# Optimization experiments

Measured on AMD Instinct MI355X. Metric: run time of the kernel, lower is better.

Reference implementation:

```python
import jax, jax.numpy as jnp
import numpy as np

B, T, P, H, D = 2, 2048, 1024, 16, 128
C = H * D  # 2048
ROPE_THETA = 10000.0


def setup_inputs() -> dict:
    key = jax.random.key(0)
    ks = jax.random.split(key, 5)
    x = jax.random.normal(ks[0], (B, T, C), jnp.float32)
    w_qkv = jax.random.normal(ks[1], (C, 3 * C), jnp.float32) * 0.02  # Linear(dim, 3*dim), applied as x @ w
    w_out = jax.random.normal(ks[2], (C, C), jnp.float32) * 0.02
    past_k = jax.random.normal(ks[3], (B, H, P, D), jnp.float32)
    past_v = jax.random.normal(ks[4], (B, H, P, D), jnp.float32)
    return {"x": x, "w_qkv": w_qkv, "w_out": w_out, "past_k": past_k, "past_v": past_v}


def _rope(q, k, offset):
    # rotate-half RoPE (GPT-NeoX style), positions offset..offset+T-1
    d = q.shape[-1]
    inv_freq = 1.0 / (ROPE_THETA ** (jnp.arange(0, d, 2, dtype=jnp.float32) / d))  # [d/2]
    pos = offset + jnp.arange(q.shape[2], dtype=jnp.float32)                        # [T]
    ang = pos[:, None] * inv_freq[None, :]                                          # [T, d/2]
    cos = jnp.concatenate([jnp.cos(ang), jnp.cos(ang)], -1)[None, None]             # [1,1,T,d]
    sin = jnp.concatenate([jnp.sin(ang), jnp.sin(ang)], -1)[None, None]

    def rot_half(t):
        t1, t2 = jnp.split(t, 2, axis=-1)
        return jnp.concatenate([-t2, t1], -1)

    return q * cos + rot_half(q) * sin, k * cos + rot_half(k) * sin


def reference(x, w_qkv, w_out, past_k, past_v):
    Bv, Tv, Cv = x.shape
    Hn = past_k.shape[1]
    Dd = Cv // Hn
    # fused QKV projection
    qkv = x @ w_qkv                       # [B,T,3C]
    q, k, v = jnp.split(qkv, 3, axis=-1)  # each [B,T,C]

    def split_heads(t):
        return t.reshape(Bv, Tv, Hn, Dd).transpose(0, 2, 1, 3)  # [B,H,T,D]

    q, k, v = split_heads(q), split_heads(k), split_heads(v)
    # RoPE with offset = past length
    q, k = _rope(q, k, past_k.shape[2])
    # KV-cache concat along time axis
    k = jnp.concatenate([past_k, k], axis=2)  # [B,H,P+T,D]
    v = jnp.concatenate([past_v, v], axis=2)
    # SDPA: past_kv present -> is_causal=False, no mask (full attention)
    scale = 1.0 / jnp.sqrt(jnp.float32(Dd))
    scores = jnp.einsum('bhqd,bhkd->bhqk', q, k) * scale
    attn = jax.nn.softmax(scores, axis=-1)
    out = jnp.einsum('bhqk,bhkd->bhqd', attn, v)
    out = out.transpose(0, 2, 1, 3).reshape(Bv, Tv, Cv)
    return out @ w_out
```

## Files before the change

kernel.cpp:

```cpp
#include <hip/hip_runtime.h>
#include <stdint.h>

#define B_ 2
#define T_ 2048
#define P_ 1024
#define H_ 16
#define D_ 128
#define C_ 2048
#define S_ 3072
#define M_ 4096
#define N3_ 6144

typedef unsigned short u16;
typedef unsigned int uint32;
typedef __attribute__((ext_vector_type(8))) short short8;
typedef __attribute__((ext_vector_type(8))) __bf16 bf16x8;
typedef __attribute__((ext_vector_type(4))) float f32x4;
typedef __attribute__((ext_vector_type(16))) float f32x16;
typedef __attribute__((ext_vector_type(4))) unsigned short u16x4;
typedef __attribute__((ext_vector_type(4))) unsigned int uint4v;

static __device__ __forceinline__ float bf2f(u16 h) {
    union { unsigned int u; float f; } x; x.u = ((unsigned int)h) << 16; return x.f;
}
static __device__ __forceinline__ u16 f2bf(float f) {
    return __builtin_bit_cast(u16, (__bf16)f);
}
static __device__ __forceinline__ uint32 pkbf(float x, float y) {
    return (uint32)f2bf(x) | ((uint32)f2bf(y) << 16);
}

static __device__ __forceinline__ f32x4 mfma_bf16(short8 a, short8 b, f32x4 c) {
    return __builtin_amdgcn_mfma_f32_16x16x32_bf16(
        __builtin_bit_cast(bf16x8, a), __builtin_bit_cast(bf16x8, b), c, 0, 0, 0);
}
static __device__ __forceinline__ f32x16 mfma32(short8 a, short8 b, f32x16 c) {
    return __builtin_amdgcn_mfma_f32_32x32x16_bf16(
        __builtin_bit_cast(bf16x8, a), __builtin_bit_cast(bf16x8, b), c, 0, 0, 0);
}

typedef __attribute__((address_space(3))) unsigned int lds_u32;
typedef const __attribute__((address_space(1))) unsigned int glb_u32;
static __device__ __forceinline__ void gload_lds16(const void* g, void* l) {
    __builtin_amdgcn_global_load_lds((glb_u32*)g, (lds_u32*)l, 16, 0, 0);
}

static __device__ __forceinline__ void storeC(float* p, float v) { *p = v; }
static __device__ __forceinline__ void storeC(u16* p, float v) { *p = f2bf(v); }


__global__ void castx_kernel(const float* __restrict__ x, u16* __restrict__ Xb) {
    int idx = blockIdx.x * 256 + threadIdx.x;
    const float4 v = ((const float4*)x)[idx];
    u16x4 o;
    o.x = f2bf(v.x); o.y = f2bf(v.y); o.z = f2bf(v.z); o.w = f2bf(v.w);
    ((u16x4*)Xb)[idx] = o;
}

__global__ void wT_kernel(const float* __restrict__ W, u16* __restrict__ Wt,
                          int Ndim, int Kdim) {
    __shared__ float tile[64][65];
    const int n0 = blockIdx.x * 64, k0 = blockIdx.y * 64;
    const int tid = threadIdx.x;
#pragma unroll
    for (int i = 0; i < 16; i++) {
        int idx = tid + i * 256;
        int r = idx >> 6, c = idx & 63;
        tile[r][c] = W[(size_t)(k0 + r) * Ndim + n0 + c];
    }
    __syncthreads();
#pragma unroll
    for (int i = 0; i < 16; i++) {
        int idx = tid + i * 256;
        int r = idx >> 6, c = idx & 63;
        Wt[(size_t)(n0 + r) * Kdim + k0 + c] = f2bf(tile[c][r]);
    }
}

__global__ void rope_table_kernel(float* __restrict__ cosT, float* __restrict__ sinT) {
    int idx = blockIdx.x * 256 + threadIdx.x;
    int t = idx >> 6, d = idx & 63;
    float inv = powf(10000.0f, -(float)d * (1.0f / 64.0f));
    float ang = (float)(P_ + t) * inv;
    cosT[idx] = cosf(ang);
    sinT[idx] = sinf(ang);
}

__global__ void rope_qk_kernel(u16* __restrict__ QKVb, u16* __restrict__ Kc,
                               const float* __restrict__ cosT,
                               const float* __restrict__ sinT) {
    int idx = blockIdx.x * 256 + threadIdx.x;
    int d = idx & 63;
    int h = (idx >> 6) & 15;
    int t = (idx >> 10) & 2047;
    int b = idx >> 21;
    size_t rowoff = (size_t)(b * T_ + t) * N3_;
    float c = cosT[(t << 6) + d], s = sinT[(t << 6) + d];
    {
        u16* p1 = QKVb + rowoff + h * 128 + d;
        float x1 = bf2f(p1[0]), x2 = bf2f(p1[64]);
        p1[0]  = f2bf(x1 * c - x2 * s);
        p1[64] = f2bf(x2 * c + x1 * s);
    }
    {
        const u16* p1 = QKVb + rowoff + C_ + h * 128 + d;
        float x1 = bf2f(p1[0]), x2 = bf2f(p1[64]);
        u16* o = Kc + ((size_t)(b * H_ + h) * S_ + P_ + t) * 128 + d;
        o[0]  = f2bf(x1 * c - x2 * s);
        o[64] = f2bf(x2 * c + x1 * s);
    }
}

__global__ void pastk_kernel(const float* __restrict__ past_k, u16* __restrict__ Kc) {
    int idx = blockIdx.x * 256 + threadIdx.x;
    int d = idx & 127;
    int p = (idx >> 7) & 1023;
    int bh = idx >> 17;
    Kc[((size_t)bh * S_ + p) * 128 + d] = f2bf(past_k[idx]);
}

__global__ void vnewT_kernel(const u16* __restrict__ QKVb, u16* __restrict__ Vt) {
    __shared__ u16 tile[64][65];
    const int t0 = blockIdx.x * 64, d0 = blockIdx.y * 64, bh = blockIdx.z;
    const int b = bh >> 4, h = bh & 15;
    const int tid = threadIdx.x;
#pragma unroll
    for (int i = 0; i < 16; i++) {
        int idx = tid + i * 256;
        int r = idx >> 6, c = idx & 63;
        tile[r][c] = QKVb[(size_t)(b * T_ + t0 + r) * N3_ + 2 * C_ + h * 128 + d0 + c];
    }
    __syncthreads();
#pragma unroll
    for (int i = 0; i < 16; i++) {
        int idx = tid + i * 256;
        int r = idx >> 6, c = idx & 63;
        Vt[((size_t)bh * 128 + d0 + r) * S_ + P_ + t0 + c] = tile[c][r];
    }
}

__global__ void vpastT_kernel(const float* __restrict__ past_v, u16* __restrict__ Vt) {
    __shared__ float tile[64][65];
    const int p0 = blockIdx.x * 64, d0 = blockIdx.y * 64, bh = blockIdx.z;
    const int tid = threadIdx.x;
#pragma unroll
    for (int i = 0; i < 16; i++) {
        int idx = tid + i * 256;
        int r = idx >> 6, c = idx & 63;
        tile[r][c] = past_v[((size_t)bh * P_ + p0 + r) * 128 + d0 + c];
    }
    __syncthreads();
#pragma unroll
    for (int i = 0; i < 16; i++) {
        int idx = tid + i * 256;
        int r = idx >> 6, c = idx & 63;
        Vt[((size_t)bh * 128 + d0 + r) * S_ + p0 + c] = f2bf(tile[c][r]);
    }
}

template <typename OutT>
__global__ void __launch_bounds__(512, 1)
gemm3(const u16* __restrict__ A, const u16* __restrict__ Bt,
      OutT* __restrict__ Co, int Mdim, int Ndim, int Kdim) {
    __shared__ u16 lA[3 * 256 * 64];
    __shared__ u16 lB[3 * 128 * 64];
    const int nbx = Ndim >> 7;
    const int nwg = (Mdim >> 8) * nbx;
    int bid = blockIdx.x;
    int wg = (bid & 7) * (nwg >> 3) + (bid >> 3);
    const int bm = wg / nbx, bn = wg % nbx;
    const int m0 = bm << 8, n0 = bn << 7;
    const int tid = threadIdx.x;
    const int wave = tid >> 6, lane = tid & 63;
    const int mw = wave >> 1, nw = wave & 1;
    const int l15 = lane & 15, l4 = lane >> 4;

    f32x4 acc[4][4];
#pragma unroll
    for (int i = 0; i < 4; i++)
#pragma unroll
        for (int j = 0; j < 4; j++) acc[i][j] = (f32x4){0.f, 0.f, 0.f, 0.f};

    const u16* aSrc[4];
    const u16* bSrc[2];
#pragma unroll
    for (int i = 0; i < 4; i++) {
        int cid = i * 512 + tid;
        int r = cid >> 3, pc = cid & 7;
        aSrc[i] = A + (size_t)(m0 + r) * Kdim + ((pc ^ (r & 7)) << 3);
    }
#pragma unroll
    for (int i = 0; i < 2; i++) {
        int cid = i * 512 + tid;
        int r = cid >> 3, pc = cid & 7;
        bSrc[i] = Bt + (size_t)(n0 + r) * Kdim + ((pc ^ (r & 7)) << 3);
    }

#define STAGE3(bi, kt) do {                                                     \
    u16* _pa = lA + (bi) * 16384 + wave * 512;                                  \
    u16* _pb = lB + (bi) * 8192 + wave * 512;                                   \
    _Pragma("unroll")                                                           \
    for (int i = 0; i < 4; i++)                                                 \
        gload_lds16(aSrc[i] + (size_t)(kt) * 64, _pa + i * 4096);               \
    _Pragma("unroll")                                                           \
    for (int i = 0; i < 2; i++)                                                 \
        gload_lds16(bSrc[i] + (size_t)(kt) * 64, _pb + i * 4096);               \
} while (0)

    STAGE3(0, 0);
    STAGE3(1, 1);

    const int NT = Kdim >> 6;
    int bc = 0;
    for (int t = 0; t < NT; ++t) {
        if (t + 1 < NT) asm volatile("s_waitcnt vmcnt(6)" ::: "memory");
        else            asm volatile("s_waitcnt vmcnt(0)" ::: "memory");
        __builtin_amdgcn_s_barrier();
        asm volatile("" ::: "memory");
        if (t + 2 < NT) {
            int b2 = bc + 2; if (b2 >= 3) b2 -= 3;
            STAGE3(b2, t + 2);
        }
        const u16* la = lA + bc * 16384;
        const u16* lb = lB + bc * 8192;
        short8 af[4][2], bf[4][2];
#pragma unroll
        for (int i = 0; i < 4; i++)
#pragma unroll
            for (int kk = 0; kk < 2; kk++) {
                int r = mw * 64 + i * 16 + l15;
                int cb = (kk * 64 + l4 * 16) ^ ((r & 7) << 4);
                af[i][kk] = *(const short8*)&la[r * 64 + (cb >> 1)];
            }
#pragma unroll
        for (int j = 0; j < 4; j++)
#pragma unroll
            for (int kk = 0; kk < 2; kk++) {
                int r = nw * 64 + j * 16 + l15;
                int cb = (kk * 64 + l4 * 16) ^ ((r & 7) << 4);
                bf[j][kk] = *(const short8*)&lb[r * 64 + (cb >> 1)];
            }
        __builtin_amdgcn_s_setprio(1);
#pragma unroll
        for (int kk = 0; kk < 2; kk++)
#pragma unroll
            for (int i = 0; i < 4; i++)
#pragma unroll
                for (int j = 0; j < 4; j++)
                    acc[i][j] = mfma_bf16(af[i][kk], bf[j][kk], acc[i][j]);
        __builtin_amdgcn_s_setprio(0);
        __builtin_amdgcn_sched_barrier(0);
        bc = bc + 1; if (bc >= 3) bc = 0;
    }
#undef STAGE3

#pragma unroll
    for (int i = 0; i < 4; i++)
#pragma unroll
        for (int j = 0; j < 4; j++) {
            int row = m0 + mw * 64 + i * 16 + (l4 << 2);
            int col = n0 + nw * 64 + j * 16 + l15;
#pragma unroll
            for (int q = 0; q < 4; q++)
                storeC(&Co[(size_t)(row + q) * Ndim + col], acc[i][j][q]);
        }
}

__global__ void __launch_bounds__(256, 2)
attn_kernel(const u16* __restrict__ QKVb, const u16* __restrict__ Kc,
            const u16* __restrict__ Vt, u16* __restrict__ O) {
    __shared__ u16 ldsK[2][64 * 128];
    __shared__ u16 ldsV[2][128 * 64];

    int bid = blockIdx.x;
    int wg = (bid & 7) * 64 + (bid >> 3);
    const int qc = wg & 15;
    const int bh = wg >> 4;
    const int b = bh >> 4, h = bh & 15;
    const int tid = threadIdx.x, wave = tid >> 6, lane = tid & 63;
    const int l31 = lane & 31, hi = lane >> 5;

    const int krow = tid >> 4;
    const int kcol = (((tid & 15) << 4) ^ ((krow & 7) << 4)) >> 1;
    const int vrow = tid >> 3;
    const int vcol = (((tid & 7) << 4) ^ ((vrow & 7) << 4)) >> 1;

    const u16* Kbh = Kc + (size_t)bh * S_ * 128;
    const u16* Vbh = Vt + (size_t)bh * 128 * S_;

    const int tq = qc * 128 + wave * 32 + l31;
    short8 qf[8];
    {
        const u16* qp = QKVb + (size_t)(b * T_ + tq) * N3_ + h * 128 + hi * 8;
#pragma unroll
        for (int ks = 0; ks < 8; ks++) qf[ks] = *(const short8*)(qp + ks * 16);
    }

    f32x16 acco[4];
#pragma unroll
    for (int d = 0; d < 4; d++) acco[d] = (f32x16)(0.0f);
    float mrow = -1e30f, lrow = 0.f;
    const float sl2 = 0.08838834764831845f * 1.4426950408889634f;

#define STAGE(bufi, tt) do {                                                    \
    const int _s0 = (tt) * 64;                                                  \
    _Pragma("unroll")                                                           \
    for (int i = 0; i < 4; i++)                                                 \
        gload_lds16(Kbh + (size_t)(_s0 + krow + i * 16) * 128 + kcol,           \
                    (char*)&ldsK[bufi][0] + i * 4096 + wave * 1024);            \
    _Pragma("unroll")                                                           \
    for (int i = 0; i < 4; i++)                                                 \
        gload_lds16(Vbh + (size_t)(vrow + i * 32) * S_ + _s0 + vcol,            \
                    (char*)&ldsV[bufi][0] + i * 4096 + wave * 1024);            \
} while (0)

    STAGE(0, 0);
    __syncthreads();

    const int swz = (l31 & 7) << 4;

    for (int t = 0; t < S_ / 64; ++t) {
        const int cur = t & 1;
        if (t < S_ / 64 - 1) STAGE(cur ^ 1, t + 1);

        const u16* Kl = ldsK[cur];
        const u16* Vl = ldsV[cur];

        f32x16 p0 = (f32x16)(0.0f), p1 = (f32x16)(0.0f);
        __builtin_amdgcn_s_setprio(1);
#pragma unroll
        for (int ks = 0; ks < 8; ks++) {
            const int cidx = (((ks * 32 + hi * 16) ^ swz) >> 1);
            short8 k0 = *(const short8*)&Kl[(l31 << 7) + cidx];
            short8 k1 = *(const short8*)&Kl[((32 + l31) << 7) + cidx];
            p0 = mfma32(k0, qf[ks], p0);
            p1 = mfma32(k1, qf[ks], p1);
        }
        __builtin_amdgcn_s_setprio(0);

        float pm = fmaxf(p0[0], p0[1]);
#pragma unroll
        for (int r = 2; r < 16; r++) pm = fmaxf(pm, p0[r]);
#pragma unroll
        for (int r = 0; r < 16; r++) pm = fmaxf(pm, p1[r]);
        pm = fmaxf(pm, __shfl_xor(pm, 32));
        float pmS = pm * sl2;
        if (!__all(pmS <= mrow + 8.0f)) {
            float mn = fmaxf(mrow, pmS);
            float fac = exp2f(mrow - mn);
            mrow = mn;
            lrow *= fac;
#pragma unroll
            for (int d = 0; d < 4; d++)
#pragma unroll
                for (int r = 0; r < 16; r++) acco[d][r] *= fac;
        }
        float sum = 0.f;
#pragma unroll
        for (int r = 0; r < 16; r++) { p0[r] = exp2f(fmaf(p0[r], sl2, -mrow)); sum += p0[r]; }
#pragma unroll
        for (int r = 0; r < 16; r++) { p1[r] = exp2f(fmaf(p1[r], sl2, -mrow)); sum += p1[r]; }
        sum += __shfl_xor(sum, 32);
        lrow += sum;

        uint32 w[4][4];
#define PACK_HALF(pp, kh, ksout) do {                                           \
    uint32 A0 = pkbf(pp[(kh)*8 + 0], pp[(kh)*8 + 1]);                           \
    uint32 A1 = pkbf(pp[(kh)*8 + 2], pp[(kh)*8 + 3]);                           \
    uint32 B0 = pkbf(pp[(kh)*8 + 4], pp[(kh)*8 + 5]);                           \
    uint32 B1 = pkbf(pp[(kh)*8 + 6], pp[(kh)*8 + 7]);                           \
    uint32 sA0 = __shfl_xor(A0, 32), sA1 = __shfl_xor(A1, 32);                  \
    uint32 sB0 = __shfl_xor(B0, 32), sB1 = __shfl_xor(B1, 32);                  \
    w[ksout][0] = hi ? sB0 : A0;                                                \
    w[ksout][1] = hi ? sB1 : A1;                                                \
    w[ksout][2] = hi ? B0 : sA0;                                                \
    w[ksout][3] = hi ? B1 : sA1;                                                \
} while (0)
        PACK_HALF(p0, 0, 0);
        PACK_HALF(p0, 1, 1);
        PACK_HALF(p1, 0, 2);
        PACK_HALF(p1, 1, 3);
#undef PACK_HALF

        __builtin_amdgcn_s_setprio(1);
#pragma unroll
        for (int ks = 0; ks < 4; ks++) {
            uint4v pw = {w[ks][0], w[ks][1], w[ks][2], w[ks][3]};
            short8 pf = __builtin_bit_cast(short8, pw);
            const int cidx = (((ks * 32 + hi * 16) ^ swz) >> 1);
#pragma unroll
            for (int dblk = 0; dblk < 4; dblk++) {
                short8 vf = *(const short8*)&Vl[((dblk * 32 + l31) << 6) + cidx];
                acco[dblk] = mfma32(vf, pf, acco[dblk]);
            }
        }
        __builtin_amdgcn_s_setprio(0);

        __syncthreads();
    }
#undef STAGE

    float rl = 1.0f / lrow;
    u16* Op = O + (size_t)(b * T_ + tq) * C_ + h * 128;
#pragma unroll
    for (int dblk = 0; dblk < 4; dblk++)
#pragma unroll
        for (int j = 0; j < 4; j++) {
            u16x4 o;
            o.x = f2bf(acco[dblk][4 * j + 0] * rl);
            o.y = f2bf(acco[dblk][4 * j + 1] * rl);
            o.z = f2bf(acco[dblk][4 * j + 2] * rl);
            o.w = f2bf(acco[dblk][4 * j + 3] * rl);
            *(u16x4*)(Op + dblk * 32 + j * 8 + hi * 4) = o;
        }
}


extern "C" void kernel_launch(void* const* d_in, const int* in_sizes, int n_in,
                              void* d_out, int out_size, void* d_ws, size_t ws_size,
                              hipStream_t stream) {
    const float* x      = (const float*)d_in[0];
    const float* w_qkv  = (const float*)d_in[1];
    const float* w_out  = (const float*)d_in[2];
    const float* past_k = (const float*)d_in[3];
    const float* past_v = (const float*)d_in[4];
    float* out = (float*)d_out;

    char* ws = (char*)d_ws;
    u16* Xb    = (u16*)(ws);
    u16* Wqkvt = (u16*)(ws + 16777216);
    u16* Woutt = (u16*)(ws + 41943040);
    u16* QKVb  = (u16*)(ws + 50331648);
    u16* Kc    = (u16*)(ws + 100663296);
    u16* Vt    = (u16*)(ws + 125829120);
    u16* O     = (u16*)(ws + 150994944);
    float* cosT = (float*)(ws + 167772160);
    float* sinT = (float*)(ws + 168296448);

    castx_kernel<<<(M_ * C_ / 4) / 256, 256, 0, stream>>>(x, Xb);
    wT_kernel<<<dim3(N3_ / 64, C_ / 64), 256, 0, stream>>>(w_qkv, Wqkvt, N3_, C_);
    wT_kernel<<<dim3(C_ / 64, C_ / 64), 256, 0, stream>>>(w_out, Woutt, C_, C_);
    rope_table_kernel<<<(T_ * 64) / 256, 256, 0, stream>>>(cosT, sinT);

    gemm3<u16><<<(M_ / 256) * (N3_ / 128), 512, 0, stream>>>(Xb, Wqkvt, QKVb, M_, N3_, C_);

    rope_qk_kernel<<<(B_ * T_ * H_ * 64) / 256, 256, 0, stream>>>(QKVb, Kc, cosT, sinT);
    pastk_kernel<<<(B_ * H_ * P_ * D_) / 256, 256, 0, stream>>>(past_k, Kc);
    vnewT_kernel<<<dim3(T_ / 64, 2, B_ * H_), 256, 0, stream>>>(QKVb, Vt);
    vpastT_kernel<<<dim3(P_ / 64, 2, B_ * H_), 256, 0, stream>>>(past_v, Vt);

    attn_kernel<<<512, 256, 0, stream>>>(QKVb, Kc, Vt, O);

    gemm3<float><<<(M_ / 256) * (C_ / 128), 512, 0, stream>>>(O, Woutt, out, M_, C_, C_);
}
```

Measured before the change: 394.0 us.

## Process two 32-row query tiles per wave in attention, halving block size

The attention kernel now runs 128 threads per block, and each wave handles 64 query rows as two 32-row tiles (A and B). Each K and V fragment read from LDS therefore feeds twice as many MFMAs, and the loads are restaged so two waves cover the same 64-key tile. The softmax max is computed with a max3 tree, the exp sums use four partial accumulators, and bf16 packing uses the v_cvt_pk_bf16_f32 instruction. The cost is roughly double the register pressure (two sets of accumulators and Q fragments) and fewer waves per block and per CU, which reduces latency hiding.

Measured after the change: 439.1 us. 11.4% more time.

```diff
diff --git a/kernel.cpp b/kernel.cpp
--- a/kernel.cpp
+++ b/kernel.cpp
@@ -26,9 +26,12 @@
 static __device__ __forceinline__ u16 f2bf(float f) {
     return __builtin_bit_cast(u16, (__bf16)f);
 }
-static __device__ __forceinline__ uint32 pkbf(float x, float y) {
-    return (uint32)f2bf(x) | ((uint32)f2bf(y) << 16);
-}
+static __device__ __forceinline__ uint32 cvtpk(float lo, float hi) {
+    uint32 r;
+    asm("v_cvt_pk_bf16_f32 %0, %1, %2" : "=v"(r) : "v"(lo), "v"(hi));
+    return r;
+}
+#define MAX3(a, b, c) fmaxf(fmaxf((a), (b)), (c))
 
 static __device__ __forceinline__ f32x4 mfma_bf16(short8 a, short8 b, f32x4 c) {
     return __builtin_amdgcn_mfma_f32_16x16x32_bf16(
@@ -266,7 +269,7 @@
         }
 }
 
-__global__ void __launch_bounds__(256, 2)
+__global__ void __launch_bounds__(128, 1)
 attn_kernel(const u16* __restrict__ QKVb, const u16* __restrict__ Kc,
             const u16* __restrict__ Vt, u16* __restrict__ O) {
     __shared__ u16 ldsK[2][64 * 128];
@@ -281,43 +284,112 @@
     const int l31 = lane & 31, hi = lane >> 5;
 
     const int krow = tid >> 4;
-    const int kcol = (((tid & 15) << 4) ^ ((krow & 7) << 4)) >> 1;
+    const int kcol = (((tid & 15) << 4) ^ (krow << 4)) >> 1;
     const int vrow = tid >> 3;
     const int vcol = (((tid & 7) << 4) ^ ((vrow & 7) << 4)) >> 1;
 
     const u16* Kbh = Kc + (size_t)bh * S_ * 128;
     const u16* Vbh = Vt + (size_t)bh * 128 * S_;
 
-    const int tq = qc * 128 + wave * 32 + l31;
-    short8 qf[8];
+    const int tqA = qc * 128 + wave * 64 + l31;
+    short8 qfA[8], qfB[8];
     {
-        const u16* qp = QKVb + (size_t)(b * T_ + tq) * N3_ + h * 128 + hi * 8;
-#pragma unroll
-        for (int ks = 0; ks < 8; ks++) qf[ks] = *(const short8*)(qp + ks * 16);
-    }
-
-    f32x16 acco[4];
-#pragma unroll
-    for (int d = 0; d < 4; d++) acco[d] = (f32x16)(0.0f);
-    float mrow = -1e30f, lrow = 0.f;
+        const u16* qpA = QKVb + (size_t)(b * T_ + tqA) * N3_ + h * 128 + hi * 8;
+        const u16* qpB = qpA + (size_t)32 * N3_;
+#pragma unroll
+        for (int ks = 0; ks < 8; ks++) {
+            qfA[ks] = *(const short8*)(qpA + ks * 16);
+            qfB[ks] = *(const short8*)(qpB + ks * 16);
+        }
+    }
+
+    f32x16 accoA[4], accoB[4];
+#pragma unroll
+    for (int d = 0; d < 4; d++) { accoA[d] = (f32x16)(0.0f); accoB[d] = (f32x16)(0.0f); }
+    float mrowA = -1e30f, lrowA = 0.f, mrowB = -1e30f, lrowB = 0.f;
     const float sl2 = 0.08838834764831845f * 1.4426950408889634f;
 
 #define STAGE(bufi, tt) do {                                                    \
     const int _s0 = (tt) * 64;                                                  \
     _Pragma("unroll")                                                           \
-    for (int i = 0; i < 4; i++)                                                 \
-        gload_lds16(Kbh + (size_t)(_s0 + krow + i * 16) * 128 + kcol,           \
-                    (char*)&ldsK[bufi][0] + i * 4096 + wave * 1024);            \
+    for (int i = 0; i < 8; i++)                                                 \
+        gload_lds16(Kbh + (size_t)(_s0 + krow + i * 8) * 128 + kcol,            \
+                    (char*)&ldsK[bufi][0] + i * 2048 + wave * 1024);            \
     _Pragma("unroll")                                                           \
-    for (int i = 0; i < 4; i++)                                                 \
-        gload_lds16(Vbh + (size_t)(vrow + i * 32) * S_ + _s0 + vcol,            \
-                    (char*)&ldsV[bufi][0] + i * 4096 + wave * 1024);            \
+    for (int i = 0; i < 8; i++)                                                 \
+        gload_lds16(Vbh + (size_t)(vrow + i * 16) * S_ + _s0 + vcol,            \
+                    (char*)&ldsV[bufi][0] + i * 2048 + wave * 1024);            \
 } while (0)
 
     STAGE(0, 0);
     __syncthreads();
 
     const int swz = (l31 & 7) << 4;
+
+#define SOFTMAX_PACK(P0, P1, MR, LR, ACC, W) do {                               \
+    float t0_ = MAX3(P0[0], P0[1], P0[2]);                                      \
+    float t1_ = MAX3(P0[3], P0[4], P0[5]);                                      \
+    float t2_ = MAX3(P0[6], P0[7], P0[8]);                                      \
+    float t3_ = MAX3(P0[9], P0[10], P0[11]);                                    \
+    float t4_ = MAX3(P0[12], P0[13], P0[14]);                                   \
+    float t5_ = MAX3(P0[15], P1[0], P1[1]);                                     \
+    float t6_ = MAX3(P1[2], P1[3], P1[4]);                                      \
+    float t7_ = MAX3(P1[5], P1[6], P1[7]);                                      \
+    float t8_ = MAX3(P1[8], P1[9], P1[10]);                                     \
+    float t9_ = MAX3(P1[11], P1[12], P1[13]);                                   \
+    float u0_ = MAX3(t0_, t1_, t2_);                                            \
+    float u1_ = MAX3(t3_, t4_, t5_);                                            \
+    float u2_ = MAX3(t6_, t7_, t8_);                                            \
+    float u3_ = MAX3(t9_, P1[14], P1[15]);                                      \
+    float pm_ = fmaxf(MAX3(u0_, u1_, u2_), u3_);                                \
+    pm_ = fmaxf(pm_, __shfl_xor(pm_, 32));                                      \
+    float pmS_ = pm_ * sl2;                                                     \
+    if (!__all(pmS_ <= (MR) + 8.0f)) {                                          \
+        float mn_ = fmaxf((MR), pmS_);                                          \
+        float fac_ = exp2f((MR) - mn_);                                         \
+        (MR) = mn_;                                                             \
+        (LR) *= fac_;                                                           \
+        _Pragma("unroll")                                                       \
+        for (int d_ = 0; d_ < 4; d_++)                                          \
+            _Pragma("unroll")                                                   \
+            for (int r_ = 0; r_ < 16; r_++) ACC[d_][r_] *= fac_;                \
+    }                                                                           \
+    float s0_ = 0.f, s1_ = 0.f, s2_ = 0.f, s3_ = 0.f;                           \
+    _Pragma("unroll")                                                           \
+    for (int r_ = 0; r_ < 16; r_ += 4) {                                        \
+        P0[r_ + 0] = exp2f(fmaf(P0[r_ + 0], sl2, -(MR))); s0_ += P0[r_ + 0];    \
+        P0[r_ + 1] = exp2f(fmaf(P0[r_ + 1], sl2, -(MR))); s1_ += P0[r_ + 1];    \
+        P0[r_ + 2] = exp2f(fmaf(P0[r_ + 2], sl2, -(MR))); s2_ += P0[r_ + 2];    \
+        P0[r_ + 3] = exp2f(fmaf(P0[r_ + 3], sl2, -(MR))); s3_ += P0[r_ + 3];    \
+    }                                                                           \
+    _Pragma("unroll")                                                           \
+    for (int r_ = 0; r_ < 16; r_ += 4) {                                        \
+        P1[r_ + 0] = exp2f(fmaf(P1[r_ + 0], sl2, -(MR))); s0_ += P1[r_ + 0];    \
+        P1[r_ + 1] = exp2f(fmaf(P1[r_ + 1], sl2, -(MR))); s1_ += P1[r_ + 1];    \
+        P1[r_ + 2] = exp2f(fmaf(P1[r_ + 2], sl2, -(MR))); s2_ += P1[r_ + 2];    \
+        P1[r_ + 3] = exp2f(fmaf(P1[r_ + 3], sl2, -(MR))); s3_ += P1[r_ + 3];    \
+    }                                                                           \
+    float sum_ = (s0_ + s1_) + (s2_ + s3_);                                     \
+    sum_ += __shfl_xor(sum_, 32);                                               \
+    (LR) += sum_;                                                               \
+    PACK_HALF(P0, 0, 0, W);                                                     \
+    PACK_HALF(P0, 1, 1, W);                                                     \
+    PACK_HALF(P1, 0, 2, W);                                                     \
+    PACK_HALF(P1, 1, 3, W);                                                     \
+} while (0)
+
+#define PACK_HALF(pp, kh, ksout, W) do {                                        \
+    uint32 A0 = cvtpk(pp[(kh)*8 + 0], pp[(kh)*8 + 1]);                          \
+    uint32 A1 = cvtpk(pp[(kh)*8 + 2], pp[(kh)*8 + 3]);                          \
+    uint32 B0 = cvtpk(pp[(kh)*8 + 4], pp[(kh)*8 + 5]);                          \
+    uint32 B1 = cvtpk(pp[(kh)*8 + 6], pp[(kh)*8 + 7]);                          \
+    uint32 sA0 = __shfl_xor(A0, 32), sA1 = __shfl_xor(A1, 32);                  \
+    uint32 sB0 = __shfl_xor(B0, 32), sB1 = __shfl_xor(B1, 32);                  \
+    W[ksout][0] = hi ? sB0 : A0;                                                \
+    W[ksout][1] = hi ? sB1 : A1;                                                \
+    W[ksout][2] = hi ? B0 : sA0;                                                \
+    W[ksout][3] = hi ? B1 : sA1;                                                \
+} while (0)
 
     for (int t = 0; t < S_ / 64; ++t) {
         const int cur = t & 1;
@@ -326,72 +398,38 @@
         const u16* Kl = ldsK[cur];
         const u16* Vl = ldsV[cur];
 
-        f32x16 p0 = (f32x16)(0.0f), p1 = (f32x16)(0.0f);
+        f32x16 pA0 = (f32x16)(0.0f), pA1 = (f32x16)(0.0f);
+        f32x16 pB0 = (f32x16)(0.0f), pB1 = (f32x16)(0.0f);
         __builtin_amdgcn_s_setprio(1);
 #pragma unroll
         for (int ks = 0; ks < 8; ks++) {
             const int cidx = (((ks * 32 + hi * 16) ^ swz) >> 1);
             short8 k0 = *(const short8*)&Kl[(l31 << 7) + cidx];
             short8 k1 = *(const short8*)&Kl[((32 + l31) << 7) + cidx];
-            p0 = mfma32(k0, qf[ks], p0);
-            p1 = mfma32(k1, qf[ks], p1);
+            pA0 = mfma32(k0, qfA[ks], pA0);
+            pA1 = mfma32(k1, qfA[ks], pA1);
+            pB0 = mfma32(k0, qfB[ks], pB0);
+            pB1 = mfma32(k1, qfB[ks], pB1);
         }
         __builtin_amdgcn_s_setprio(0);
 
-        float pm = fmaxf(p0[0], p0[1]);
-#pragma unroll
-        for (int r = 2; r < 16; r++) pm = fmaxf(pm, p0[r]);
-#pragma unroll
-        for (int r = 0; r < 16; r++) pm = fmaxf(pm, p1[r]);
-        pm = fmaxf(pm, __shfl_xor(pm, 32));
-        float pmS = pm * sl2;
-        if (!__all(pmS <= mrow + 8.0f)) {
-            float mn = fmaxf(mrow, pmS);
-            float fac = exp2f(mrow - mn);
-            mrow = mn;
-            lrow *= fac;
-#pragma unroll
-            for (int d = 0; d < 4; d++)
-#pragma unroll
-                for (int r = 0; r < 16; r++) acco[d][r] *= fac;
-        }
-        float sum = 0.f;
-#pragma unroll
-        for (int r = 0; r < 16; r++) { p0[r] = exp2f(fmaf(p0[r], sl2, -mrow)); sum += p0[r]; }
-#pragma unroll
-        for (int r = 0; r < 16; r++) { p1[r] = exp2f(fmaf(p1[r], sl2, -mrow)); sum += p1[r]; }
-        sum += __shfl_xor(sum, 32);
-        lrow += sum;
-
-        uint32 w[4][4];
-#define PACK_HALF(pp, kh, ksout) do {                                           \
-    uint32 A0 = pkbf(pp[(kh)*8 + 0], pp[(kh)*8 + 1]);                           \
-    uint32 A1 = pkbf(pp[(kh)*8 + 2], pp[(kh)*8 + 3]);                           \
-    uint32 B0 = pkbf(pp[(kh)*8 + 4], pp[(kh)*8 + 5]);                           \
-    uint32 B1 = pkbf(pp[(kh)*8 + 6], pp[(kh)*8 + 7]);                           \
-    uint32 sA0 = __shfl_xor(A0, 32), sA1 = __shfl_xor(A1, 32);                  \
-    uint32 sB0 = __shfl_xor(B0, 32), sB1 = __shfl_xor(B1, 32);                  \
-    w[ksout][0] = hi ? sB0 : A0;                                                \
-    w[ksout][1] = hi ? sB1 : A1;                                                \
-    w[ksout][2] = hi ? B0 : sA0;                                                \
-    w[ksout][3] = hi ? B1 : sA1;                                                \
-} while (0)
-        PACK_HALF(p0, 0, 0);
-        PACK_HALF(p0, 1, 1);
-        PACK_HALF(p1, 0, 2);
-        PACK_HALF(p1, 1, 3);
-#undef PACK_HALF
+        uint32 wA[4][4], wB[4][4];
+        SOFTMAX_PACK(pA0, pA1, mrowA, lrowA, accoA, wA);
+        SOFTMAX_PACK(pB0, pB1, mrowB, lrowB, accoB, wB);
 
         __builtin_amdgcn_s_setprio(1);
 #pragma unroll
         for (int ks = 0; ks < 4; ks++) {
-            uint4v pw = {w[ks][0], w[ks][1], w[ks][2], w[ks][3]};
-            short8 pf = __builtin_bit_cast(short8, pw);
+            uint4v pwA = {wA[ks][0], wA[ks][1], wA[ks][2], wA[ks][3]};
+            uint4v pwB = {wB[ks][0], wB[ks][1], wB[ks][2], wB[ks][3]};
+            short8 pfA = __builtin_bit_cast(short8, pwA);
+            short8 pfB = __builtin_bit_cast(short8, pwB);
             const int cidx = (((ks * 32 + hi * 16) ^ swz) >> 1);
 #pragma unroll
             for (int dblk = 0; dblk < 4; dblk++) {
                 short8 vf = *(const short8*)&Vl[((dblk * 32 + l31) << 6) + cidx];
-                acco[dblk] = mfma32(vf, pf, acco[dblk]);
+                accoA[dblk] = mfma32(vf, pfA, accoA[dblk]);
+                accoB[dblk] = mfma32(vf, pfB, accoB[dblk]);
             }
         }
         __builtin_amdgcn_s_setprio(0);
@@ -399,19 +437,27 @@
         __syncthreads();
     }
 #undef STAGE
-
-    float rl = 1.0f / lrow;
-    u16* Op = O + (size_t)(b * T_ + tq) * C_ + h * 128;
+#undef SOFTMAX_PACK
+#undef PACK_HALF
+
+    float rlA = 1.0f / lrowA, rlB = 1.0f / lrowB;
+    u16* OpA = O + (size_t)(b * T_ + tqA) * C_ + h * 128;
+    u16* OpB = OpA + (size_t)32 * C_;
 #pragma unroll
     for (int dblk = 0; dblk < 4; dblk++)
 #pragma unroll
         for (int j = 0; j < 4; j++) {
-            u16x4 o;
-            o.x = f2bf(acco[dblk][4 * j + 0] * rl);
-            o.y = f2bf(acco[dblk][4 * j + 1] * rl);
-            o.z = f2bf(acco[dblk][4 * j + 2] * rl);
-            o.w = f2bf(acco[dblk][4 * j + 3] * rl);
-            *(u16x4*)(Op + dblk * 32 + j * 8 + hi * 4) = o;
+            u16x4 oA, oB;
+            oA.x = f2bf(accoA[dblk][4 * j + 0] * rlA);
+            oA.y = f2bf(accoA[dblk][4 * j + 1] * rlA);
+            oA.z = f2bf(accoA[dblk][4 * j + 2] * rlA);
+            oA.w = f2bf(accoA[dblk][4 * j + 3] * rlA);
+            *(u16x4*)(OpA + dblk * 32 + j * 8 + hi * 4) = oA;
+            oB.x = f2bf(accoB[dblk][4 * j + 0] * rlB);
+            oB.y = f2bf(accoB[dblk][4 * j + 1] * rlB);
+            oB.z = f2bf(accoB[dblk][4 * j + 2] * rlB);
+            oB.w = f2bf(accoB[dblk][4 * j + 3] * rlB);
+            *(u16x4*)(OpB + dblk * 32 + j * 8 + hi * 4) = oB;
         }
 }
 
@@ -449,7 +495,7 @@
     vnewT_kernel<<<dim3(T_ / 64, 2, B_ * H_), 256, 0, stream>>>(QKVb, Vt);
     vpastT_kernel<<<dim3(P_ / 64, 2, B_ * H_), 256, 0, stream>>>(past_v, Vt);
 
-    attn_kernel<<<512, 256, 0, stream>>>(QKVb, Kc, Vt, O);
+    attn_kernel<<<512, 128, 0, stream>>>(QKVb, Kc, Vt, O);
 
     gemm3<float><<<(M_ / 256) * (C_ / 128), 512, 0, stream>>>(O, Woutt, out, M_, C_, C_);
 }
```
